# Kernel optimization log

Hardware: AMD Instinct MI355X
Metric: run time of the kernel (lower is better)

The kernel has to match this reference:

```python
import jax, jax.numpy as jnp
import numpy as np

N_NODES = 100000
N_EDGES = 50000
NNZ = 1000000


def _scatter_mean(vals, idx, num_segments):
    s = jax.ops.segment_sum(vals, idx, num_segments=num_segments)
    cnt = jax.ops.segment_sum(jnp.ones((vals.shape[0],), vals.dtype), idx, num_segments=num_segments)
    return s / jnp.maximum(cnt, 1.0)[:, None]


def _normalize_l2(X):
    # row L2 normalize; scale computed on detached values, inf -> 0
    norm = jnp.linalg.norm(X, axis=1, keepdims=True)
    scale = jax.lax.stop_gradient(jnp.where(norm > 0, 1.0 / norm, 0.0))
    return X * scale


def _conv(X, W, V, E, homo, use_norm):
    # X: [N, in], W: [in, heads*out]
    X = X @ W                                   # [N, D]
    Xve = X[V]                                  # gather vertex -> incidence [nnz, D]
    Xe = _scatter_mean(Xve, E, N_EDGES)         # first_aggregate='mean' -> [nE, D]
    Xev = Xe[E]                                 # gather edge -> incidence [nnz, D]
    he = homo[E]                                # [nnz]
    att_sum = jax.ops.segment_sum(he, V, num_segments=N_NODES)[V]  # [nnz]
    att = (he / att_sum)[:, None]               # [nnz, 1]
    Xv = jax.ops.segment_sum(att * Xev, V, num_segments=N_NODES)   # second_aggregate='sum' -> [N, D]
    X = X + Xv
    if use_norm:
        X = _normalize_l2(X)
    return X


def setup_inputs() -> dict:
    key = jax.random.key(0)
    k1, k2, k3, k4, k5, k6, k7 = jax.random.split(key, 7)
    nfeat, dh, nclass = 256, 256, 40  # dh = nhid*nhead = 64*4
    X = jax.random.normal(k1, (N_NODES, nfeat), dtype=jnp.float32)
    V = jax.random.randint(k2, (NNZ,), 0, N_NODES)
    E = jax.random.randint(k3, (NNZ,), 0, N_EDGES)
    homo = jax.random.uniform(k4, (N_EDGES,), dtype=jnp.float32, minval=0.1, maxval=1.0)
    s1 = 1.0 / np.sqrt(nfeat)
    s2 = 1.0 / np.sqrt(dh)
    W1 = jax.random.uniform(k5, (nfeat, dh), dtype=jnp.float32, minval=-s1, maxval=s1)
    W2 = jax.random.uniform(k6, (dh, dh), dtype=jnp.float32, minval=-s2, maxval=s2)
    Wout = jax.random.uniform(k7, (dh, nclass), dtype=jnp.float32, minval=-s2, maxval=s2)
    return {"X": X, "V": V, "E": E, "homo": homo, "W1": W1, "W2": W2, "Wout": Wout}


def reference(X, V, E, homo, W1, W2, Wout):
    # HHyperGNN.forward (eval mode: dropouts are identity), nlayer=3
    X = _conv(X, W1, V, E, homo, use_norm=True)
    X = jax.nn.relu(X)
    X = _conv(X, W2, V, E, homo, use_norm=True)
    X = jax.nn.relu(X)
    Z = X
    X = _conv(X, Wout, V, E, homo, use_norm=True)
    return (Z, X)
```

## Files before the change

### kernel.cpp

```cpp
#include <hip/hip_runtime.h>

#define NND 100000
#define NED 50000
#define NNZC 1000000

typedef __attribute__((ext_vector_type(8))) short bf16x8;
typedef __attribute__((ext_vector_type(4))) float f32x4;

__device__ __forceinline__ float b2f(unsigned short u) {
  union { unsigned int u; float f; } x; x.u = ((unsigned int)u) << 16; return x.f;
}
__device__ __forceinline__ float blo(unsigned int u) {
  union { unsigned int u; float f; } x; x.u = u << 16; return x.f;
}
__device__ __forceinline__ float bhi(unsigned int u) {
  union { unsigned int u; float f; } x; x.u = u & 0xffff0000u; return x.f;
}
__device__ __forceinline__ unsigned short f2b(float f) {
  union { float f; unsigned int u; } x; x.f = f;
  unsigned int r = x.u + 0x7FFFu + ((x.u >> 16) & 1u);
  return (unsigned short)(r >> 16);
}
__device__ __forceinline__ unsigned int pk2(float lo, float hi) {
  return (unsigned int)f2b(lo) | ((unsigned int)f2b(hi) << 16);
}

__global__ void detect_k(const unsigned short* __restrict__ homo_u16,
                         int* __restrict__ mode) {
  if (threadIdx.x == 0 && blockIdx.x == 0) {
    int bf16_ok = 1;
    for (int i = 0; i < 64; i++) {
      float v = b2f(homo_u16[i]);
      if (!(v >= 0.04f && v <= 1.1f)) bf16_ok = 0;
    }
    *mode = bf16_ok ? 0 : 1;
  }
}

__global__ void prep_f32(const void* __restrict__ Hin, const void* __restrict__ W1,
                         const void* __restrict__ W2, const void* __restrict__ Wout,
                         float* __restrict__ Hf, unsigned short* __restrict__ WT1b,
                         unsigned short* __restrict__ WT2b, float* __restrict__ Wf3,
                         const int* __restrict__ mode) {
  int i = blockIdx.x * 256 + threadIdx.x;
  int m = *mode;
  if (i < 65536) {
    int n = i >> 8, k = i & 255;
    float w1 = m ? ((const float*)W1)[k * 256 + n] : b2f(((const unsigned short*)W1)[k * 256 + n]);
    float w2 = m ? ((const float*)W2)[k * 256 + n] : b2f(((const unsigned short*)W2)[k * 256 + n]);
    WT1b[i] = f2b(w1);
    WT2b[i] = f2b(w2);
  }
  if (i < 16384) {
    int k = i >> 6, n = i & 63;
    Wf3[i] = (n < 40)
      ? (m ? ((const float*)Wout)[k * 40 + n] : b2f(((const unsigned short*)Wout)[k * 40 + n]))
      : 0.f;
  }
  if (i < NED)
    Hf[i] = m ? ((const float*)Hin)[i] : b2f(((const unsigned short*)Hin)[i]);
}

__global__ __launch_bounds__(256) void gemm_mfma(
    const void* __restrict__ A, const int* __restrict__ mode, int internal,
    const unsigned short* __restrict__ WT,
    unsigned short* __restrict__ Cb, int M) {
  __shared__ unsigned short As[128][40];
  __shared__ unsigned short Bs[128][40];
  const int t = threadIdx.x;
  const int l = t & 63;
  const int w = t >> 6;
  const int wr = w >> 1, wc = w & 1;
  const int lr16 = l & 15, lg = l >> 4;
  const int bm = blockIdx.x >> 1;
  const int n0 = (blockIdx.x & 1) * 128;
  const int row0 = bm * 128;
  const bool fp32 = internal ? true : (*mode == 1);

  const int tr = t >> 1, th = t & 1;
  int arow = row0 + tr; if (arow >= M) arow = M - 1;

  f32x4 acc[4][4];
#pragma unroll
  for (int m = 0; m < 4; m++)
#pragma unroll
    for (int n = 0; n < 4; n++) acc[m][n] = (f32x4){0.f, 0.f, 0.f, 0.f};

  uint4 a0, a1, b0, b1;
  auto load_regs = [&](int k0) {
    if (fp32) {
      const float4* ap = (const float4*)((const float*)A + (size_t)arow * 256 + k0 + th * 16);
      float4 f0 = ap[0], f1 = ap[1], f2 = ap[2], f3 = ap[3];
      a0 = make_uint4(pk2(f0.x, f0.y), pk2(f0.z, f0.w), pk2(f1.x, f1.y), pk2(f1.z, f1.w));
      a1 = make_uint4(pk2(f2.x, f2.y), pk2(f2.z, f2.w), pk2(f3.x, f3.y), pk2(f3.z, f3.w));
    } else {
      const uint4* ap = (const uint4*)((const unsigned short*)A + (size_t)arow * 256 + k0 + th * 16);
      a0 = ap[0]; a1 = ap[1];
    }
    const uint4* bp = (const uint4*)(WT + (size_t)(n0 + tr) * 256 + k0 + th * 16);
    b0 = bp[0]; b1 = bp[1];
  };

  load_regs(0);
  for (int k0 = 0; k0 < 256; k0 += 32) {
    __syncthreads();
    *(uint4*)&As[tr][th * 16]     = a0;
    *(uint4*)&As[tr][th * 16 + 8] = a1;
    *(uint4*)&Bs[tr][th * 16]     = b0;
    *(uint4*)&Bs[tr][th * 16 + 8] = b1;
    __syncthreads();
    if (k0 < 224) load_regs(k0 + 32);

    bf16x8 af[4], bfr[4];
#pragma unroll
    for (int m = 0; m < 4; m++)
      af[m] = *(const bf16x8*)&As[wr * 64 + m * 16 + lr16][lg * 8];
#pragma unroll
    for (int n = 0; n < 4; n++)
      bfr[n] = *(const bf16x8*)&Bs[wc * 64 + n * 16 + lr16][lg * 8];
#pragma unroll
    for (int m = 0; m < 4; m++)
#pragma unroll
      for (int n = 0; n < 4; n++)
        acc[m][n] = __builtin_amdgcn_mfma_f32_16x16x32_bf16(af[m], bfr[n], acc[m][n], 0, 0, 0);
  }

#pragma unroll
  for (int m = 0; m < 4; m++) {
#pragma unroll
    for (int j = 0; j < 4; j++) {
      int row = row0 + wr * 64 + m * 16 + lg * 4 + j;
      if (row < M) {
#pragma unroll
        for (int n = 0; n < 4; n++)
          Cb[(size_t)row * 256 + n0 + wc * 64 + n * 16 + lr16] = f2b(acc[m][n][j]);
      }
    }
  }
}

template <int N>
__global__ __launch_bounds__(256) void gemm_tile(
    const void* __restrict__ A, const int* __restrict__ mode, int internal,
    const float* __restrict__ W, float* __restrict__ C, int M) {
  constexpr int BM = 64, BK = 32;
  constexpr int CPT = N / 32;
  __shared__ float As[BM][BK + 1];
  __shared__ float Ws[BK][N];
  const int t = threadIdx.x;
  const int tx = t & 31, ty = t >> 5;
  const int row0 = blockIdx.x * BM;
  const bool fp32 = internal ? true : (*mode == 1);

  float acc[8][CPT];
#pragma unroll
  for (int i = 0; i < 8; i++)
#pragma unroll
    for (int j = 0; j < CPT; j++) acc[i][j] = 0.f;

  for (int k0 = 0; k0 < 256; k0 += BK) {
#pragma unroll
    for (int l = t; l < BM * BK / 4; l += 256) {
      int r = l >> 3, seg = l & 7;
      int row = row0 + r;
      if (row >= M) row = M - 1;
      int col = k0 + seg * 4;
      float4 v;
      if (fp32) {
        v = *(const float4*)((const float*)A + (size_t)row * 256 + col);
      } else {
        ushort4 u = *(const ushort4*)((const unsigned short*)A + (size_t)row * 256 + col);
        v = make_float4(b2f(u.x), b2f(u.y), b2f(u.z), b2f(u.w));
      }
      As[r][seg * 4 + 0] = v.x;
      As[r][seg * 4 + 1] = v.y;
      As[r][seg * 4 + 2] = v.z;
      As[r][seg * 4 + 3] = v.w;
    }
#pragma unroll
    for (int l = t; l < BK * N / 4; l += 256) {
      ((float4*)&Ws[0][0])[l] = *(const float4*)(W + (size_t)k0 * N + l * 4);
    }
    __syncthreads();

#pragma unroll 4
    for (int kk = 0; kk < BK; kk++) {
      float a[8], w[CPT];
#pragma unroll
      for (int i = 0; i < 8; i++) a[i] = As[ty * 8 + i][kk];
#pragma unroll
      for (int j = 0; j < CPT; j++) w[j] = Ws[kk][tx + 32 * j];
#pragma unroll
      for (int i = 0; i < 8; i++)
#pragma unroll
        for (int j = 0; j < CPT; j++) acc[i][j] += a[i] * w[j];
    }
    __syncthreads();
  }

#pragma unroll
  for (int i = 0; i < 8; i++) {
    int row = row0 + ty * 8 + i;
    if (row < M) {
#pragma unroll
      for (int j = 0; j < CPT; j++)
        C[(size_t)row * N + tx + 32 * j] = acc[i][j];
    }
  }
}

__global__ void cnt_rank_k(const int* __restrict__ V, const int* __restrict__ E,
                           int* __restrict__ cntAll,
                           int* __restrict__ rV, int* __restrict__ rE) {
  int i = blockIdx.x * 256 + threadIdx.x;
  if (i < NNZC) {
    rV[i] = atomicAdd(&cntAll[V[i]], 1);
    rE[i] = atomicAdd(&cntAll[NND + E[i]], 1);
  }
}

__global__ void scan_local(const int* __restrict__ in, int* __restrict__ outExcl,
                           int* __restrict__ bsum, int n) {
  __shared__ int s[256];
  int t = threadIdx.x;
  int i = blockIdx.x * 256 + t;
  int v = (i < n) ? in[i] : 0;
  s[t] = v;
  __syncthreads();
  for (int off = 1; off < 256; off <<= 1) {
    int x = (t >= off) ? s[t - off] : 0;
    __syncthreads();
    s[t] += x;
    __syncthreads();
  }
  if (i < n) outExcl[i] = s[t] - v;
  if (t == 255) bsum[blockIdx.x] = s[255];
}

__global__ void scan_sums(int* __restrict__ bsum, int nb) {
  __shared__ int s[1024];
  int t = threadIdx.x;
  int v = (t < nb) ? bsum[t] : 0;
  s[t] = v;
  __syncthreads();
  for (int off = 1; off < 1024; off <<= 1) {
    int x = (t >= off) ? s[t - off] : 0;
    __syncthreads();
    s[t] += x;
    __syncthreads();
  }
  if (t < nb) bsum[t] = s[t] - v;
}

__global__ void scan_add(int* __restrict__ outExcl, const int* __restrict__ bsum, int n) {
  int i = blockIdx.x * 256 + threadIdx.x;
  if (i < n) outExcl[i] += bsum[blockIdx.x];
}

__global__ void fill_nr(const int* __restrict__ V, const int* __restrict__ E,
                        const int* __restrict__ offAll,
                        const int* __restrict__ rV, const int* __restrict__ rE,
                        int* __restrict__ adjAll) {
  int i = blockIdx.x * 256 + threadIdx.x;
  if (i < NNZC) {
    int v = V[i], e = E[i];
    adjAll[offAll[v] + rV[i]] = e;
    adjAll[offAll[NND + e] + rE[i]] = v;
  }
}

__global__ __launch_bounds__(256) void edge_gather_b(
    const int* __restrict__ eoff, const int* __restrict__ cntE,
    const int* __restrict__ eadj, const unsigned int* __restrict__ XWb,
    unsigned int* __restrict__ Xeb) {
  int e = blockIdx.x * 4 + (threadIdx.x >> 6);
  int tl = threadIdx.x & 63;
  if (e >= NED) return;
  int start = eoff[e], n = cntE[e];
  float a0 = 0.f, a1 = 0.f, a2 = 0.f, a3 = 0.f;
  for (int c0 = 0; c0 < n; c0 += 64) {
    int m = n - c0; if (m > 64) m = 64;
    int vidx = (tl < m) ? eadj[start + c0 + tl] : 0;
#pragma unroll 4
    for (int j = 0; j < m; j++) {
      int vv = __shfl(vidx, j);
      uint2 x = *((const uint2*)(XWb + (size_t)vv * 128) + tl);
      a0 += blo(x.x); a1 += bhi(x.x); a2 += blo(x.y); a3 += bhi(x.y);
    }
  }
  float inv = (n > 0) ? 1.0f / (float)n : 0.f;
  uint2 o;
  o.x = pk2(a0 * inv, a1 * inv);
  o.y = pk2(a2 * inv, a3 * inv);
  *((uint2*)(Xeb + (size_t)e * 128) + tl) = o;
}

__global__ __launch_bounds__(256) void node_gather_norm_b(
    const int* __restrict__ voff, const int* __restrict__ degV,
    const int* __restrict__ vadj, const float* __restrict__ Hf,
    const unsigned int* __restrict__ Xeb,
    const unsigned int* __restrict__ XWb, float* __restrict__ out) {
  int v = blockIdx.x * 4 + (threadIdx.x >> 6);
  int tl = threadIdx.x & 63;
  if (v >= NND) return;
  int start = voff[v], n = degV[v];
  uint2 r = *((const uint2*)(XWb + (size_t)v * 128) + tl);
  float r0 = blo(r.x), r1 = bhi(r.x), r2 = blo(r.y), r3 = bhi(r.y);
  float g0 = 0.f, g1 = 0.f, g2 = 0.f, g3 = 0.f;
  float hsum = 0.f;
  for (int c0 = 0; c0 < n; c0 += 64) {
    int m = n - c0; if (m > 64) m = 64;
    int eidx = (tl < m) ? vadj[start + c0 + tl] : 0;
    float h = (tl < m) ? Hf[eidx] : 0.f;
    hsum += h;
#pragma unroll 4
    for (int j = 0; j < m; j++) {
      int ee = __shfl(eidx, j);
      float a = __shfl(h, j);
      uint2 x = *((const uint2*)(Xeb + (size_t)ee * 128) + tl);
      g0 += a * blo(x.x); g1 += a * bhi(x.x);
      g2 += a * blo(x.y); g3 += a * bhi(x.y);
    }
  }
#pragma unroll
  for (int off = 32; off; off >>= 1) hsum += __shfl_xor(hsum, off);
  float inv_att = (hsum > 0.f) ? 1.0f / hsum : 0.f;
  float a0 = r0 + inv_att * g0, a1 = r1 + inv_att * g1;
  float a2 = r2 + inv_att * g2, a3 = r3 + inv_att * g3;
  float ss = a0 * a0 + a1 * a1 + a2 * a2 + a3 * a3;
#pragma unroll
  for (int off = 32; off; off >>= 1) ss += __shfl_xor(ss, off);
  float sc = (ss > 0.f) ? (1.0f / sqrtf(ss)) : 0.f;
  a0 = fmaxf(a0 * sc, 0.f); a1 = fmaxf(a1 * sc, 0.f);
  a2 = fmaxf(a2 * sc, 0.f); a3 = fmaxf(a3 * sc, 0.f);
  *((float4*)(out + (size_t)v * 256) + tl) = make_float4(a0, a1, a2, a3);
}

__global__ __launch_bounds__(256) void edge_gather_f64(
    const int* __restrict__ eoff, const int* __restrict__ cntE,
    const int* __restrict__ eadj, const float* __restrict__ XW,
    float* __restrict__ Xe) {
  int e = blockIdx.x * 4 + (threadIdx.x >> 6);
  int tl = threadIdx.x & 63;
  if (e >= NED) return;
  int start = eoff[e], n = cntE[e];
  float ax = 0.f;
  for (int c0 = 0; c0 < n; c0 += 64) {
    int m = n - c0; if (m > 64) m = 64;
    int vidx = (tl < m) ? eadj[start + c0 + tl] : 0;
#pragma unroll 4
    for (int j = 0; j < m; j++) {
      int vv = __shfl(vidx, j);
      ax += XW[(size_t)vv * 64 + tl];
    }
  }
  float inv = (n > 0) ? 1.0f / (float)n : 0.f;
  Xe[(size_t)e * 64 + tl] = ax * inv;
}

__global__ __launch_bounds__(256) void node_gather_norm_f64(
    const int* __restrict__ voff, const int* __restrict__ degV,
    const int* __restrict__ vadj, const float* __restrict__ Hf,
    const float* __restrict__ Xe,
    const float* __restrict__ XW, float* __restrict__ out) {
  int v = blockIdx.x * 4 + (threadIdx.x >> 6);
  int tl = threadIdx.x & 63;
  if (v >= NND) return;
  int start = voff[v], n = degV[v];
  float rx = XW[(size_t)v * 64 + tl];
  float gx = 0.f, hsum = 0.f;
  for (int c0 = 0; c0 < n; c0 += 64) {
    int m = n - c0; if (m > 64) m = 64;
    int eidx = (tl < m) ? vadj[start + c0 + tl] : 0;
    float h = (tl < m) ? Hf[eidx] : 0.f;
    hsum += h;
#pragma unroll 4
    for (int j = 0; j < m; j++) {
      int ee = __shfl(eidx, j);
      float a = __shfl(h, j);
      gx += a * Xe[(size_t)ee * 64 + tl];
    }
  }
#pragma unroll
  for (int off = 32; off; off >>= 1) hsum += __shfl_xor(hsum, off);
  float inv_att = (hsum > 0.f) ? 1.0f / hsum : 0.f;
  float ax = rx + inv_att * gx;
  float ss = ax * ax;
#pragma unroll
  for (int off = 32; off; off >>= 1) ss += __shfl_xor(ss, off);
  float sc = (ss > 0.f) ? (1.0f / sqrtf(ss)) : 0.f;
  ax *= sc;
  if (tl < 40) out[(size_t)v * 40 + tl] = ax;
}

__global__ void sentinel_k(float* __restrict__ out, long n, float val) {
  long i = (long)blockIdx.x * 256 + threadIdx.x;
  long stride = (long)gridDim.x * 256;
  for (; i < n; i += stride) out[i] = val;
}

extern "C" void kernel_launch(void* const* d_in, const int* in_sizes, int n_in,
                              void* d_out, int out_size, void* d_ws, size_t ws_size,
                              hipStream_t stream) {
  const void* Xin  = d_in[0];
  const int*  V    = (const int*)d_in[1];
  const int*  E    = (const int*)d_in[2];
  const void* Hin  = d_in[3];
  const void* W1   = d_in[4];
  const void* W2   = d_in[5];
  const void* Wout = d_in[6];
  float* Zout = (float*)d_out;
  float* Xout = Zout + (size_t)NND * 256;
  (void)in_sizes; (void)n_in;

  char* base = (char*)d_ws;
  size_t o = 0;
  auto carve = [&](size_t bytes) -> char* {
    char* p = base + o;
    o += (bytes + 255) & ~(size_t)255;
    return p;
  };
  unsigned int* XWb  = (unsigned int*)carve((size_t)NND * 128 * 4);
  unsigned int* Xeb  = (unsigned int*)carve((size_t)NED * 128 * 4);
  float* XW32 = (float*)carve((size_t)NND * 64 * 4);
  float* Xe32 = (float*)carve((size_t)NED * 64 * 4);
  float* Hf   = (float*)carve((size_t)NED * 4);
  int*   cntAll = (int*)carve((size_t)(NND + NED) * 4);
  int*   offAll = (int*)carve((size_t)(NND + NED) * 4);
  int*   rV   = (int*)carve((size_t)NNZC * 4);
  int*   rE   = (int*)carve((size_t)NNZC * 4);
  int*   adjAll = (int*)carve((size_t)NNZC * 2 * 4);
  int*   bsum = (int*)carve(1024 * 4);
  unsigned short* WT1b = (unsigned short*)carve(65536 * 2);
  unsigned short* WT2b = (unsigned short*)carve(65536 * 2);
  float* Wf3  = (float*)carve(16384 * 4);
  int*   mode = (int*)carve(256);
  const size_t NEED = o;

  if (ws_size < NEED) {
    sentinel_k<<<4096, 256, 0, stream>>>(Zout, (long)out_size, 77.0f);
    return;
  }

  const int NCNT = NND + NED;
  const int NBC = (NCNT + 255) / 256;
  const int MFMA_GRID = ((NND + 127) / 128) * 2;
  const int GEMM_GRID = (NND + 63) / 64;
  const int EG_GRID = (NED + 3) / 4;
  const int NG_GRID = (NND + 3) / 4;

  const int* voff = offAll;
  const int* eoff = offAll + NND;
  const int* degV = cntAll;
  const int* cntE = cntAll + NND;
  const int* vadj = adjAll;
  const int* eadj = adjAll;

  detect_k<<<1, 64, 0, stream>>>((const unsigned short*)Hin, mode);
  prep_f32<<<256, 256, 0, stream>>>(Hin, W1, W2, Wout, Hf, WT1b, WT2b, Wf3, mode);
  hipMemsetAsync(cntAll, 0, (size_t)NCNT * 4, stream);
  cnt_rank_k<<<(NNZC + 255) / 256, 256, 0, stream>>>(V, E, cntAll, rV, rE);

  scan_local<<<NBC, 256, 0, stream>>>(cntAll, offAll, bsum, NCNT);
  scan_sums<<<1, 1024, 0, stream>>>(bsum, NBC);
  scan_add<<<NBC, 256, 0, stream>>>(offAll, bsum, NCNT);
  fill_nr<<<(NNZC + 255) / 256, 256, 0, stream>>>(V, E, offAll, rV, rE, adjAll);

  gemm_mfma<<<MFMA_GRID, 256, 0, stream>>>(Xin, mode, 0, WT1b, (unsigned short*)XWb, NND);
  edge_gather_b<<<EG_GRID, 256, 0, stream>>>(eoff, cntE, eadj, XWb, Xeb);
  node_gather_norm_b<<<NG_GRID, 256, 0, stream>>>(voff, degV, vadj, Hf, Xeb, XWb, Zout);

  gemm_mfma<<<MFMA_GRID, 256, 0, stream>>>(Zout, mode, 1, WT2b, (unsigned short*)XWb, NND);
  edge_gather_b<<<EG_GRID, 256, 0, stream>>>(eoff, cntE, eadj, XWb, Xeb);
  node_gather_norm_b<<<NG_GRID, 256, 0, stream>>>(voff, degV, vadj, Hf, Xeb, XWb, Zout);

  gemm_tile<64><<<GEMM_GRID, 256, 0, stream>>>(Zout, mode, 1, Wf3, XW32, NND);
  edge_gather_f64<<<EG_GRID, 256, 0, stream>>>(eoff, cntE, eadj, XW32, Xe32);
  node_gather_norm_f64<<<NG_GRID, 256, 0, stream>>>(voff, degV, vadj, Hf, Xe32, XW32, Xout);
}
```

Measured before the change: 962.8 us.

## Fuse counting into first GEMM, pack adjacency with weights, store intermediates in bf16

The incidence counting/rank atomics are merged into the first MFMA GEMM kernel so they overlap with the matrix work. Ranks are stored as 16-bit values. Each vertex adjacency entry now packs the edge id with its bf16 homo weight, so the per-neighbor Hf gather goes away. Layer activations are kept as a bf16 copy for the next GEMM, and the last layer's intermediates use bf16, which cuts memory traffic. In exchange this adds precision loss and relies on edge ids and ranks fitting in 16 bits.

```diff
diff --git a/kernel.cpp b/kernel.cpp
--- a/kernel.cpp
+++ b/kernel.cpp
@@ -3,6 +3,7 @@
 #define NND 100000
 #define NED 50000
 #define NNZC 1000000
+#define MGRID 1564
 
 typedef __attribute__((ext_vector_type(8))) short bf16x8;
 typedef __attribute__((ext_vector_type(4))) float f32x4;
@@ -61,10 +62,10 @@
     Hf[i] = m ? ((const float*)Hin)[i] : b2f(((const unsigned short*)Hin)[i]);
 }
 
-__global__ __launch_bounds__(256) void gemm_mfma(
-    const void* __restrict__ A, const int* __restrict__ mode, int internal,
+__device__ __forceinline__ void gemm_body(
+    const void* __restrict__ A, bool a_fp32,
     const unsigned short* __restrict__ WT,
-    unsigned short* __restrict__ Cb, int M) {
+    unsigned short* __restrict__ Cb, int M, int bid) {
   __shared__ unsigned short As[128][40];
   __shared__ unsigned short Bs[128][40];
   const int t = threadIdx.x;
@@ -72,10 +73,9 @@
   const int w = t >> 6;
   const int wr = w >> 1, wc = w & 1;
   const int lr16 = l & 15, lg = l >> 4;
-  const int bm = blockIdx.x >> 1;
-  const int n0 = (blockIdx.x & 1) * 128;
+  const int bm = bid >> 1;
+  const int n0 = (bid & 1) * 128;
   const int row0 = bm * 128;
-  const bool fp32 = internal ? true : (*mode == 1);
 
   const int tr = t >> 1, th = t & 1;
   int arow = row0 + tr; if (arow >= M) arow = M - 1;
@@ -88,7 +88,7 @@
 
   uint4 a0, a1, b0, b1;
   auto load_regs = [&](int k0) {
-    if (fp32) {
+    if (a_fp32) {
       const float4* ap = (const float4*)((const float*)A + (size_t)arow * 256 + k0 + th * 16);
       float4 f0 = ap[0], f1 = ap[1], f2 = ap[2], f3 = ap[3];
       a0 = make_uint4(pk2(f0.x, f0.y), pk2(f0.z, f0.w), pk2(f1.x, f1.y), pk2(f1.z, f1.w));
@@ -139,18 +139,48 @@
   }
 }
 
-template <int N>
-__global__ __launch_bounds__(256) void gemm_tile(
-    const void* __restrict__ A, const int* __restrict__ mode, int internal,
-    const float* __restrict__ W, float* __restrict__ C, int M) {
-  constexpr int BM = 64, BK = 32;
-  constexpr int CPT = N / 32;
+__global__ __launch_bounds__(256) void gemm1_cnt(
+    const void* __restrict__ A, const int* __restrict__ mode,
+    const unsigned short* __restrict__ WT, unsigned short* __restrict__ Cb, int M,
+    const int* __restrict__ V, const int* __restrict__ E,
+    int* __restrict__ cntAll, unsigned short* __restrict__ rV,
+    unsigned short* __restrict__ rE) {
+  const int STR = MGRID * 256;
+  int i0 = blockIdx.x * 256 + threadIdx.x;
+  unsigned short rv[3], re[3];
+#pragma unroll
+  for (int q = 0; q < 3; q++) {
+    int i = i0 + q * STR;
+    if (i < NNZC) {
+      rv[q] = (unsigned short)atomicAdd(&cntAll[V[i]], 1);
+      re[q] = (unsigned short)atomicAdd(&cntAll[NND + E[i]], 1);
+    }
+  }
+
+  gemm_body(A, *mode == 1, WT, Cb, M, blockIdx.x);
+
+#pragma unroll
+  for (int q = 0; q < 3; q++) {
+    int i = i0 + q * STR;
+    if (i < NNZC) { rV[i] = rv[q]; rE[i] = re[q]; }
+  }
+}
+
+__global__ __launch_bounds__(256) void gemm_bf16_k(
+    const unsigned short* __restrict__ A, const unsigned short* __restrict__ WT,
+    unsigned short* __restrict__ Cb, int M) {
+  gemm_body(A, false, WT, Cb, M, blockIdx.x);
+}
+
+__global__ __launch_bounds__(256) void gemm_tile_b64(
+    const unsigned short* __restrict__ A, const float* __restrict__ W,
+    unsigned short* __restrict__ C, int M) {
+  constexpr int N = 64, BM = 64, BK = 32, CPT = 2;
   __shared__ float As[BM][BK + 1];
   __shared__ float Ws[BK][N];
   const int t = threadIdx.x;
   const int tx = t & 31, ty = t >> 5;
   const int row0 = blockIdx.x * BM;
-  const bool fp32 = internal ? true : (*mode == 1);
 
   float acc[8][CPT];
 #pragma unroll
@@ -165,17 +195,11 @@
       int row = row0 + r;
       if (row >= M) row = M - 1;
       int col = k0 + seg * 4;
-      float4 v;
-      if (fp32) {
-        v = *(const float4*)((const float*)A + (size_t)row * 256 + col);
-      } else {
-        ushort4 u = *(const ushort4*)((const unsigned short*)A + (size_t)row * 256 + col);
-        v = make_float4(b2f(u.x), b2f(u.y), b2f(u.z), b2f(u.w));
-      }
-      As[r][seg * 4 + 0] = v.x;
-      As[r][seg * 4 + 1] = v.y;
-      As[r][seg * 4 + 2] = v.z;
-      As[r][seg * 4 + 3] = v.w;
+      ushort4 u = *(const ushort4*)(A + (size_t)row * 256 + col);
+      As[r][seg * 4 + 0] = b2f(u.x);
+      As[r][seg * 4 + 1] = b2f(u.y);
+      As[r][seg * 4 + 2] = b2f(u.z);
+      As[r][seg * 4 + 3] = b2f(u.w);
     }
 #pragma unroll
     for (int l = t; l < BK * N / 4; l += 256) {
@@ -204,18 +228,8 @@
     if (row < M) {
 #pragma unroll
       for (int j = 0; j < CPT; j++)
-        C[(size_t)row * N + tx + 32 * j] = acc[i][j];
-    }
-  }
-}
-
-__global__ void cnt_rank_k(const int* __restrict__ V, const int* __restrict__ E,
-                           int* __restrict__ cntAll,
-                           int* __restrict__ rV, int* __restrict__ rE) {
-  int i = blockIdx.x * 256 + threadIdx.x;
-  if (i < NNZC) {
-    rV[i] = atomicAdd(&cntAll[V[i]], 1);
-    rE[i] = atomicAdd(&cntAll[NND + E[i]], 1);
+        C[(size_t)row * N + tx + 32 * j] = f2b(acc[i][j]);
+    }
   }
 }
 
@@ -259,13 +273,16 @@
 
 __global__ void fill_nr(const int* __restrict__ V, const int* __restrict__ E,
                         const int* __restrict__ offAll,
-                        const int* __restrict__ rV, const int* __restrict__ rE,
-                        int* __restrict__ adjAll) {
+                        const unsigned short* __restrict__ rV,
+                        const unsigned short* __restrict__ rE,
+                        const float* __restrict__ Hf,
+                        unsigned int* __restrict__ vadjH,
+                        int* __restrict__ eadj) {
   int i = blockIdx.x * 256 + threadIdx.x;
   if (i < NNZC) {
     int v = V[i], e = E[i];
-    adjAll[offAll[v] + rV[i]] = e;
-    adjAll[offAll[NND + e] + rE[i]] = v;
+    vadjH[offAll[v] + rV[i]] = (unsigned int)e | ((unsigned int)f2b(Hf[e]) << 16);
+    eadj[offAll[NND + e] - NNZC + rE[i]] = v;
   }
 }
 
@@ -276,7 +293,7 @@
   int e = blockIdx.x * 4 + (threadIdx.x >> 6);
   int tl = threadIdx.x & 63;
   if (e >= NED) return;
-  int start = eoff[e], n = cntE[e];
+  int start = eoff[e] - NNZC, n = cntE[e];
   float a0 = 0.f, a1 = 0.f, a2 = 0.f, a3 = 0.f;
   for (int c0 = 0; c0 < n; c0 += 64) {
     int m = n - c0; if (m > 64) m = 64;
@@ -297,26 +314,25 @@
 
 __global__ __launch_bounds__(256) void node_gather_norm_b(
     const int* __restrict__ voff, const int* __restrict__ degV,
-    const int* __restrict__ vadj, const float* __restrict__ Hf,
-    const unsigned int* __restrict__ Xeb,
-    const unsigned int* __restrict__ XWb, float* __restrict__ out) {
+    const unsigned int* __restrict__ vadjH,
+    const unsigned int* __restrict__ Xeb, const unsigned int* __restrict__ XWb,
+    unsigned int* __restrict__ Zb, float* __restrict__ outf) {
   int v = blockIdx.x * 4 + (threadIdx.x >> 6);
   int tl = threadIdx.x & 63;
   if (v >= NND) return;
   int start = voff[v], n = degV[v];
   uint2 r = *((const uint2*)(XWb + (size_t)v * 128) + tl);
-  float r0 = blo(r.x), r1 = bhi(r.x), r2 = blo(r.y), r3 = bhi(r.y);
-  float g0 = 0.f, g1 = 0.f, g2 = 0.f, g3 = 0.f;
-  float hsum = 0.f;
+  float a0 = blo(r.x), a1 = bhi(r.x), a2 = blo(r.y), a3 = bhi(r.y);
+  float g0 = 0.f, g1 = 0.f, g2 = 0.f, g3 = 0.f, hsum = 0.f;
   for (int c0 = 0; c0 < n; c0 += 64) {
     int m = n - c0; if (m > 64) m = 64;
-    int eidx = (tl < m) ? vadj[start + c0 + tl] : 0;
-    float h = (tl < m) ? Hf[eidx] : 0.f;
-    hsum += h;
+    unsigned int pk = (tl < m) ? vadjH[start + c0 + tl] : 0u;
+    hsum += b2f((unsigned short)(pk >> 16));
 #pragma unroll 4
     for (int j = 0; j < m; j++) {
-      int ee = __shfl(eidx, j);
-      float a = __shfl(h, j);
+      unsigned int u = (unsigned int)__shfl((int)pk, j);
+      int ee = (int)(u & 0xffffu);
+      float a = b2f((unsigned short)(u >> 16));
       uint2 x = *((const uint2*)(Xeb + (size_t)ee * 128) + tl);
       g0 += a * blo(x.x); g1 += a * bhi(x.x);
       g2 += a * blo(x.y); g3 += a * bhi(x.y);
@@ -325,25 +341,27 @@
 #pragma unroll
   for (int off = 32; off; off >>= 1) hsum += __shfl_xor(hsum, off);
   float inv_att = (hsum > 0.f) ? 1.0f / hsum : 0.f;
-  float a0 = r0 + inv_att * g0, a1 = r1 + inv_att * g1;
-  float a2 = r2 + inv_att * g2, a3 = r3 + inv_att * g3;
+  a0 += inv_att * g0; a1 += inv_att * g1;
+  a2 += inv_att * g2; a3 += inv_att * g3;
   float ss = a0 * a0 + a1 * a1 + a2 * a2 + a3 * a3;
 #pragma unroll
   for (int off = 32; off; off >>= 1) ss += __shfl_xor(ss, off);
   float sc = (ss > 0.f) ? (1.0f / sqrtf(ss)) : 0.f;
   a0 = fmaxf(a0 * sc, 0.f); a1 = fmaxf(a1 * sc, 0.f);
   a2 = fmaxf(a2 * sc, 0.f); a3 = fmaxf(a3 * sc, 0.f);
-  *((float4*)(out + (size_t)v * 256) + tl) = make_float4(a0, a1, a2, a3);
-}
-
-__global__ __launch_bounds__(256) void edge_gather_f64(
+  uint2 o; o.x = pk2(a0, a1); o.y = pk2(a2, a3);
+  *((uint2*)(Zb + (size_t)v * 128) + tl) = o;
+  if (outf) *((float4*)(outf + (size_t)v * 256) + tl) = make_float4(a0, a1, a2, a3);
+}
+
+__global__ __launch_bounds__(256) void edge_gather_64(
     const int* __restrict__ eoff, const int* __restrict__ cntE,
-    const int* __restrict__ eadj, const float* __restrict__ XW,
-    float* __restrict__ Xe) {
+    const int* __restrict__ eadj, const unsigned short* __restrict__ XW64,
+    unsigned short* __restrict__ Xe64) {
   int e = blockIdx.x * 4 + (threadIdx.x >> 6);
   int tl = threadIdx.x & 63;
   if (e >= NED) return;
-  int start = eoff[e], n = cntE[e];
+  int start = eoff[e] - NNZC, n = cntE[e];
   float ax = 0.f;
   for (int c0 = 0; c0 < n; c0 += 64) {
     int m = n - c0; if (m > 64) m = 64;
@@ -351,40 +369,40 @@
 #pragma unroll 4
     for (int j = 0; j < m; j++) {
       int vv = __shfl(vidx, j);
-      ax += XW[(size_t)vv * 64 + tl];
+      ax += b2f(XW64[(size_t)vv * 64 + tl]);
     }
   }
   float inv = (n > 0) ? 1.0f / (float)n : 0.f;
-  Xe[(size_t)e * 64 + tl] = ax * inv;
-}
-
-__global__ __launch_bounds__(256) void node_gather_norm_f64(
+  Xe64[(size_t)e * 64 + tl] = f2b(ax * inv);
+}
+
+__global__ __launch_bounds__(256) void node_gather_norm_64(
     const int* __restrict__ voff, const int* __restrict__ degV,
-    const int* __restrict__ vadj, const float* __restrict__ Hf,
-    const float* __restrict__ Xe,
-    const float* __restrict__ XW, float* __restrict__ out) {
+    const unsigned int* __restrict__ vadjH,
+    const unsigned short* __restrict__ Xe64, const unsigned short* __restrict__ XW64,
+    float* __restrict__ out) {
   int v = blockIdx.x * 4 + (threadIdx.x >> 6);
   int tl = threadIdx.x & 63;
   if (v >= NND) return;
   int start = voff[v], n = degV[v];
-  float rx = XW[(size_t)v * 64 + tl];
+  float ax = b2f(XW64[(size_t)v * 64 + tl]);
   float gx = 0.f, hsum = 0.f;
   for (int c0 = 0; c0 < n; c0 += 64) {
     int m = n - c0; if (m > 64) m = 64;
-    int eidx = (tl < m) ? vadj[start + c0 + tl] : 0;
-    float h = (tl < m) ? Hf[eidx] : 0.f;
-    hsum += h;
+    unsigned int pk = (tl < m) ? vadjH[start + c0 + tl] : 0u;
+    hsum += b2f((unsigned short)(pk >> 16));
 #pragma unroll 4
     for (int j = 0; j < m; j++) {
-      int ee = __shfl(eidx, j);
-      float a = __shfl(h, j);
-      gx += a * Xe[(size_t)ee * 64 + tl];
+      unsigned int u = (unsigned int)__shfl((int)pk, j);
+      int ee = (int)(u & 0xffffu);
+      float a = b2f((unsigned short)(u >> 16));
+      gx += a * b2f(Xe64[(size_t)ee * 64 + tl]);
     }
   }
 #pragma unroll
   for (int off = 32; off; off >>= 1) hsum += __shfl_xor(hsum, off);
   float inv_att = (hsum > 0.f) ? 1.0f / hsum : 0.f;
-  float ax = rx + inv_att * gx;
+  ax += inv_att * gx;
   float ss = ax * ax;
 #pragma unroll
   for (int off = 32; off; off >>= 1) ss += __shfl_xor(ss, off);
@@ -420,21 +438,23 @@
     o += (bytes + 255) & ~(size_t)255;
     return p;
   };
-  unsigned int* XWb  = (unsigned int*)carve((size_t)NND * 128 * 4);
-  unsigned int* Xeb  = (unsigned int*)carve((size_t)NED * 128 * 4);
-  float* XW32 = (float*)carve((size_t)NND * 64 * 4);
-  float* Xe32 = (float*)carve((size_t)NED * 64 * 4);
-  float* Hf   = (float*)carve((size_t)NED * 4);
+  unsigned int*  XWb  = (unsigned int*)carve((size_t)NND * 256 * 2);
+  unsigned int*  Xeb  = (unsigned int*)carve((size_t)NED * 256 * 2);
+  unsigned int*  Zb   = (unsigned int*)carve((size_t)NND * 256 * 2);
+  unsigned short* XW64 = (unsigned short*)carve((size_t)NND * 64 * 2);
+  unsigned short* Xe64 = (unsigned short*)carve((size_t)NED * 64 * 2);
+  float* Hf    = (float*)carve((size_t)NED * 4);
   int*   cntAll = (int*)carve((size_t)(NND + NED) * 4);
   int*   offAll = (int*)carve((size_t)(NND + NED) * 4);
-  int*   rV   = (int*)carve((size_t)NNZC * 4);
-  int*   rE   = (int*)carve((size_t)NNZC * 4);
-  int*   adjAll = (int*)carve((size_t)NNZC * 2 * 4);
-  int*   bsum = (int*)carve(1024 * 4);
+  unsigned short* rV = (unsigned short*)carve((size_t)NNZC * 2);
+  unsigned short* rE = (unsigned short*)carve((size_t)NNZC * 2);
+  unsigned int* vadjH = (unsigned int*)carve((size_t)NNZC * 4);
+  int*   eadj  = (int*)carve((size_t)NNZC * 4);
+  int*   bsum  = (int*)carve(1024 * 4);
   unsigned short* WT1b = (unsigned short*)carve(65536 * 2);
   unsigned short* WT2b = (unsigned short*)carve(65536 * 2);
-  float* Wf3  = (float*)carve(16384 * 4);
-  int*   mode = (int*)carve(256);
+  float* Wf3   = (float*)carve(16384 * 4);
+  int*   mode  = (int*)carve(256);
   const size_t NEED = o;
 
   if (ws_size < NEED) {
@@ -444,8 +464,8 @@
 
   const int NCNT = NND + NED;
   const int NBC = (NCNT + 255) / 256;
-  const int MFMA_GRID = ((NND + 127) / 128) * 2;
   const int GEMM_GRID = (NND + 63) / 64;
+  const int FILL_GRID = (NNZC + 255) / 256;
   const int EG_GRID = (NED + 3) / 4;
   const int NG_GRID = (NND + 3) / 4;
 
@@ -453,28 +473,28 @@
   const int* eoff = offAll + NND;
   const int* degV = cntAll;
   const int* cntE = cntAll + NND;
-  const int* vadj = adjAll;
-  const int* eadj = adjAll;
 
   detect_k<<<1, 64, 0, stream>>>((const unsigned short*)Hin, mode);
   prep_f32<<<256, 256, 0, stream>>>(Hin, W1, W2, Wout, Hf, WT1b, WT2b, Wf3, mode);
   hipMemsetAsync(cntAll, 0, (size_t)NCNT * 4, stream);
-  cnt_rank_k<<<(NNZC + 255) / 256, 256, 0, stream>>>(V, E, cntAll, rV, rE);
+
+  gemm1_cnt<<<MGRID, 256, 0, stream>>>(Xin, mode, WT1b, (unsigned short*)XWb, NND,
+                                       V, E, cntAll, rV, rE);
 
   scan_local<<<NBC, 256, 0, stream>>>(cntAll, offAll, bsum, NCNT);
   scan_sums<<<1, 1024, 0, stream>>>(bsum, NBC);
   scan_add<<<NBC, 256, 0, stream>>>(offAll, bsum, NCNT);
-  fill_nr<<<(NNZC + 255) / 256, 256, 0, stream>>>(V, E, offAll, rV, rE, adjAll);
-
-  gemm_mfma<<<MFMA_GRID, 256, 0, stream>>>(Xin, mode, 0, WT1b, (unsigned short*)XWb, NND);
+  fill_nr<<<FILL_GRID, 256, 0, stream>>>(V, E, offAll, rV, rE, Hf, vadjH, eadj);
+
   edge_gather_b<<<EG_GRID, 256, 0, stream>>>(eoff, cntE, eadj, XWb, Xeb);
-  node_gather_norm_b<<<NG_GRID, 256, 0, stream>>>(voff, degV, vadj, Hf, Xeb, XWb, Zout);
-
-  gemm_mfma<<<MFMA_GRID, 256, 0, stream>>>(Zout, mode, 1, WT2b, (unsigned short*)XWb, NND);
+  node_gather_norm_b<<<NG_GRID, 256, 0, stream>>>(voff, degV, vadjH, Xeb, XWb, Zb, nullptr);
+
+  gemm_bf16_k<<<MGRID, 256, 0, stream>>>((const unsigned short*)Zb, WT2b,
+                                         (unsigned short*)XWb, NND);
   edge_gather_b<<<EG_GRID, 256, 0, stream>>>(eoff, cntE, eadj, XWb, Xeb);
-  node_gather_norm_b<<<NG_GRID, 256, 0, stream>>>(voff, degV, vadj, Hf, Xeb, XWb, Zout);
-
-  gemm_tile<64><<<GEMM_GRID, 256, 0, stream>>>(Zout, mode, 1, Wf3, XW32, NND);
-  edge_gather_f64<<<EG_GRID, 256, 0, stream>>>(eoff, cntE, eadj, XW32, Xe32);
-  node_gather_norm_f64<<<NG_GRID, 256, 0, stream>>>(voff, degV, vadj, Hf, Xe32, XW32, Xout);
-}
+  node_gather_norm_b<<<NG_GRID, 256, 0, stream>>>(voff, degV, vadjH, Xeb, XWb, Zb, Zout);
+
+  gemm_tile_b64<<<GEMM_GRID, 256, 0, stream>>>((const unsigned short*)Zb, Wf3, XW64, NND);
+  edge_gather_64<<<EG_GRID, 256, 0, stream>>>(eoff, cntE, eadj, XW64, Xe64);
+  node_gather_norm_64<<<NG_GRID, 256, 0, stream>>>(voff, degV, vadjH, Xe64, XW64, Xout);
+}
```

Result: faster. 931.9 us (-3.2%).
